# Kernel tuning notes

Measured on AMD Instinct MI355X. Metric: run time of the kernel, lower is better.

## Reference

```python
import jax, jax.numpy as jnp
import numpy as np

NUM_HEADS = 12
DIM = 768
HEAD_DIM = DIM // NUM_HEADS
SCALE = HEAD_DIM ** -0.5
LORA_ALPHA = 1.0


def setup_inputs() -> dict:
    key = jax.random.key(0)
    ks = jax.random.split(key, 9)
    B, H, W = 1, 64, 64
    return {
        "x": jax.random.normal(ks[0], (B, H, W, DIM), jnp.float32),
        "w_qkv": jax.random.normal(ks[1], (3 * DIM, DIM), jnp.float32) * 0.02,
        "b_qkv": jax.random.normal(ks[2], (3 * DIM,), jnp.float32) * 0.02,
        "lora_A": jax.random.normal(ks[3], (12, DIM), jnp.float32) * 0.02,
        "lora_B": jax.random.normal(ks[4], (3 * DIM, 12), jnp.float32) * 0.02,
        "w_proj": jax.random.normal(ks[5], (DIM, DIM), jnp.float32) * 0.02,
        "b_proj": jax.random.normal(ks[6], (DIM,), jnp.float32) * 0.02,
        "rel_pos_h": jax.random.normal(ks[7], (2 * H - 1, HEAD_DIM), jnp.float32) * 0.02,
        "rel_pos_w": jax.random.normal(ks[8], (2 * W - 1, HEAD_DIM), jnp.float32) * 0.02,
    }


def _get_rel_pos(size: int, rel_pos: jnp.ndarray) -> jnp.ndarray:
    # q_size == k_size and rel_pos.shape[0] == 2*size-1, so no interpolation.
    coords = jnp.arange(size)[:, None] - jnp.arange(size)[None, :] + (size - 1)
    return rel_pos[coords]  # [size, size, head_dim]


def reference(x, w_qkv, b_qkv, lora_A, lora_B, w_proj, b_proj, rel_pos_h, rel_pos_w):
    B, H, W, _ = x.shape
    N = H * W
    # LoRA qkv projection: W_eff path = base + alpha * x @ (B A)^T
    qkv = x @ w_qkv.T + b_qkv + LORA_ALPHA * ((x @ lora_A.T) @ lora_B.T)
    qkv = qkv.reshape(B, N, 3, NUM_HEADS, HEAD_DIM)
    qkv = jnp.transpose(qkv, (2, 0, 3, 1, 4)).reshape(3, B * NUM_HEADS, N, HEAD_DIM)
    q, k, v = qkv[0], qkv[1], qkv[2]
    attn = jnp.einsum('bqc,bkc->bqk', q * SCALE, k)  # [B*nh, N, N]
    # decomposed relative position bias
    Rh = _get_rel_pos(H, rel_pos_h)  # [H, H, hd]
    Rw = _get_rel_pos(W, rel_pos_w)  # [W, W, hd]
    r_q = q.reshape(B * NUM_HEADS, H, W, HEAD_DIM)
    rel_h = jnp.einsum('bhwc,hkc->bhwk', r_q, Rh)
    rel_w = jnp.einsum('bhwc,wkc->bhwk', r_q, Rw)
    attn = (attn.reshape(-1, H, W, H, W)
            + rel_h[:, :, :, :, None]
            + rel_w[:, :, :, None, :]).reshape(-1, N, N)
    attn = jax.nn.softmax(attn, axis=-1)
    out = jnp.einsum('bqk,bkc->bqc', attn, v)  # [B*nh, N, hd]
    out = out.reshape(B, NUM_HEADS, H, W, HEAD_DIM)
    out = jnp.transpose(out, (0, 2, 3, 1, 4)).reshape(B, H, W, DIM)
    return out @ w_proj.T + b_proj
```

## Files before the change

kernel.cpp:

```cpp
#include <hip/hip_runtime.h>
#include <stdint.h>


typedef __attribute__((ext_vector_type(4))) float f32x4;
typedef __attribute__((ext_vector_type(16))) float f32x16;
typedef __attribute__((ext_vector_type(4))) float fvec4;
typedef __attribute__((ext_vector_type(8))) short s16x8;
typedef __attribute__((ext_vector_type(4))) short s16x4;
typedef __attribute__((ext_vector_type(4))) unsigned u32x4;

constexpr int NH  = 12;
constexpr int HD  = 64;
constexpr int DIM = 768;
constexpr int N   = 4096;
constexpr int QKV = 2304;
constexpr float LOG2E  = 1.4426950408889634f;
constexpr float SCALE2 = 0.125f * LOG2E;

static __device__ __forceinline__ short f2bf(float f) {
  unsigned u = __builtin_bit_cast(unsigned, f);
  unsigned r = (u + 0x7FFFu + ((u >> 16) & 1u)) >> 16;
  return (short)r;
}
static __device__ __forceinline__ float bf2f(short s) {
  unsigned u = ((unsigned)(unsigned short)s) << 16;
  return __builtin_bit_cast(float, u);
}
static __device__ __forceinline__ unsigned cvt_pk_bf16(float a, float b) {
  unsigned r;
  asm("v_cvt_pk_bf16_f32 %0, %1, %2" : "=v"(r) : "v"(a), "v"(b));
  return r;
}
static __device__ __forceinline__ float ex2(float x) {
  float r;
  asm("v_exp_f32 %0, %1" : "=v"(r) : "v"(x));
  return r;
}
static __device__ __forceinline__ void gload16(const void* g, void* l) {
  __builtin_amdgcn_global_load_lds(
      (const __attribute__((address_space(1))) void*)g,
      (__attribute__((address_space(3))) void*)l, 16, 0, 0);
}

__global__ __launch_bounds__(256) void k_weff(const float* __restrict__ w_qkv,
                                              const float* __restrict__ lora_A,
                                              const float* __restrict__ lora_B,
                                              short* __restrict__ weff) {
  int e = blockIdx.x * 256 + threadIdx.x;
  if (e >= QKV * DIM) return;
  int r = e / DIM, c = e % DIM;
  float acc = w_qkv[e];
#pragma unroll
  for (int t = 0; t < 12; ++t) acc += lora_B[r * 12 + t] * lora_A[t * DIM + c];
  weff[e] = f2bf(acc);
}

__global__ __launch_bounds__(256) void k_x2bf(const float* __restrict__ x,
                                              short* __restrict__ xb) {
  int i = blockIdx.x * 256 + threadIdx.x;
  fvec4 v = *reinterpret_cast<const fvec4*>(x + (size_t)i * 4);
  s16x4 p;
  p[0] = f2bf(v[0]); p[1] = f2bf(v[1]); p[2] = f2bf(v[2]); p[3] = f2bf(v[3]);
  *reinterpret_cast<s16x4*>(xb + (size_t)i * 4) = p;
}

__global__ __launch_bounds__(256) void k_wsplit(const float* __restrict__ w,
                                                short* __restrict__ ws) {
  int r = blockIdx.y;
  int kk = blockIdx.x * 256 + threadIdx.x;
  int blk = (kk >= 1536) ? 2 : (kk >= 768 ? 1 : 0);
  int c = kk - blk * 768;
  float wv = w[(size_t)r * 768 + c];
  short hi = f2bf(wv);
  ws[(size_t)r * 2304 + kk] = (blk == 1) ? f2bf(wv - bf2f(hi)) : hi;
}

template <int KIT, int MODE, int BM>
__global__ __launch_bounds__(256) void k_gemm(const short* __restrict__ A,
                                              const short* __restrict__ B,
                                              const float* __restrict__ bias,
                                              short* __restrict__ qo,
                                              short* __restrict__ ko,
                                              short* __restrict__ vo,
                                              float* __restrict__ outf) {
  constexpr int MFR = BM / 32;
  __shared__ __align__(16) char lds[BM * 128 + 16384];
  const int tid = threadIdx.x;
  const int wave = tid >> 6, lane = tid & 63, lr = lane & 15, lg = lane >> 4;
  const int wr = wave >> 1, wc = wave & 1;
  const int i0 = blockIdx.x * BM, j0 = blockIdx.y * 128;
  const int LDA = KIT * 128;

  size_t offA[MFR], offB[4];
#pragma unroll
  for (int it = 0; it < MFR; ++it) {
    int c = it * 256 + tid;
    int row = c >> 3;
    offA[it] = (size_t)row * LDA + (((c & 7) << 4) ^ ((row & 7) << 4));
  }
#pragma unroll
  for (int it = 0; it < 4; ++it) {
    int c = it * 256 + tid;
    int row = c >> 3;
    offB[it] = (size_t)row * LDA + (((c & 7) << 4) ^ ((row & 7) << 4));
  }
  const char* Ab = (const char*)A + (size_t)i0 * LDA;
  const char* Bb = (const char*)B + (size_t)j0 * LDA;
  char* la = lds + wave * 1024;
  char* lb = lds + BM * 128 + wave * 1024;

  const int swz = (lr & 7) << 4;
  const int ab = (wr * (BM / 2) + lr) * 128 + ((lg * 16) ^ swz);
  const int bb = BM * 128 + (wc * 64 + lr) * 128 + ((lg * 16) ^ swz);

  f32x4 acc[MFR][4] = {};

  for (int kt = 0; kt < KIT; ++kt) {
    const size_t kadd = (size_t)kt * 128;
#pragma unroll
    for (int it = 0; it < MFR; ++it) gload16(Ab + kadd + offA[it], la + it * 4096);
#pragma unroll
    for (int it = 0; it < 4; ++it) gload16(Bb + kadd + offB[it], lb + it * 4096);
    __syncthreads();
#pragma unroll
    for (int ks2 = 0; ks2 < 2; ++ks2) {
      s16x8 af[MFR], bf_[4];
#pragma unroll
      for (int m = 0; m < MFR; ++m)
        af[m] = *reinterpret_cast<const s16x8*>(lds + ((ab + m * 2048) ^ (ks2 << 6)));
#pragma unroll
      for (int n = 0; n < 4; ++n)
        bf_[n] = *reinterpret_cast<const s16x8*>(lds + ((bb + n * 2048) ^ (ks2 << 6)));
#pragma unroll
      for (int m = 0; m < MFR; ++m)
#pragma unroll
        for (int n = 0; n < 4; ++n)
          acc[m][n] = __builtin_amdgcn_mfma_f32_16x16x32_bf16(af[m], bf_[n], acc[m][n], 0, 0, 0);
    }
    __syncthreads();
  }

  if constexpr (MODE == 0) {
    const int three = j0 / 768;
    const int head = ((j0 % 768) >> 6) + wc;
    short* dst = (three == 0) ? qo : ((three == 1) ? ko : vo);
#pragma unroll
    for (int n = 0; n < 4; ++n) {
      const int col = n * 16 + lr;
      const float bj = bias[j0 + wc * 64 + col];
#pragma unroll
      for (int m = 0; m < MFR; ++m)
#pragma unroll
        for (int r = 0; r < 4; ++r) {
          int i = i0 + wr * (BM / 2) + m * 16 + lg * 4 + r;
          dst[((size_t)head * N + i) * HD + col] = f2bf(acc[m][n][r] + bj);
        }
    }
  } else {
#pragma unroll
    for (int n = 0; n < 4; ++n) {
      const int j = j0 + wc * 64 + n * 16 + lr;
      const float bj = bias[j];
#pragma unroll
      for (int m = 0; m < MFR; ++m)
#pragma unroll
        for (int r = 0; r < 4; ++r) {
          int i = i0 + wr * (BM / 2) + m * 16 + lg * 4 + r;
          outf[(size_t)i * 768 + j] = acc[m][n][r] + bj;
        }
    }
  }
}

__global__ __launch_bounds__(256) void k_vT(const short* __restrict__ vg,
                                            short* __restrict__ vTg) {
  __shared__ short ts[64 * 72];
  const int tid = threadIdx.x;
  const int i0 = blockIdx.x * 64;
  const int h = blockIdx.y;
#pragma unroll
  for (int it = 0; it < 2; ++it) {
    int ch = tid + 256 * it;
    int row = ch >> 3, cc = (ch & 7) * 8;
    *reinterpret_cast<s16x8*>(&ts[row * 72 + cc]) =
        *reinterpret_cast<const s16x8*>(&vg[((size_t)h * N + i0 + row) * HD + cc]);
  }
  __syncthreads();
#pragma unroll
  for (int it = 0; it < 2; ++it) {
    int ch = tid + 256 * it;
    int c = ch >> 3, ii = (ch & 7) * 8;
    s16x8 o;
#pragma unroll
    for (int j = 0; j < 8; ++j) o[j] = ts[(ii + j) * 72 + c];
    *reinterpret_cast<s16x8*>(&vTg[((size_t)h * HD + c) * N + i0 + ii]) = o;
  }
}

__global__ __launch_bounds__(256) void k_relh(const short* __restrict__ qg,
                                              const float* __restrict__ tab,
                                              short* __restrict__ rhT) {
  __shared__ short Ts[64 * 72];
  const int tid = threadIdx.x;
  const int wave = tid >> 6, lane = tid & 63, lr = lane & 15, lg = lane >> 4;
  const int h = blockIdx.x >> 6, qh = blockIdx.x & 63;
#pragma unroll
  for (int it = 0; it < 4; ++it) {
    int e = tid + 256 * it;
    int row = e >> 4, c4 = (e & 15) * 4;
    fvec4 v = *reinterpret_cast<const fvec4*>(tab + (size_t)(qh + 63 - row) * 64 + c4);
    s16x4 p;
    p[0] = f2bf(v[0]); p[1] = f2bf(v[1]); p[2] = f2bf(v[2]); p[3] = f2bf(v[3]);
    *reinterpret_cast<s16x4*>(&Ts[row * 72 + c4]) = p;
  }
  __syncthreads();
  const size_t qrow = (size_t)h * N + qh * 64 + wave * 16 + lr;
  const s16x8 a0 = *reinterpret_cast<const s16x8*>(qg + qrow * 64 + lg * 8);
  const s16x8 a1 = *reinterpret_cast<const s16x8*>(qg + qrow * 64 + 32 + lg * 8);
  f32x4 acc[4] = {};
#pragma unroll
  for (int ks2 = 0; ks2 < 2; ++ks2)
#pragma unroll
    for (int n = 0; n < 4; ++n) {
      s16x8 b = *reinterpret_cast<const s16x8*>(&Ts[(n * 16 + lr) * 72 + ks2 * 32 + lg * 8]);
      acc[n] = __builtin_amdgcn_mfma_f32_16x16x32_bf16(ks2 ? a1 : a0, b, acc[n], 0, 0, 0);
    }
  const size_t ob = ((size_t)(h * 64 + qh)) * 4096;
#pragma unroll
  for (int n = 0; n < 4; ++n) {
    s16x4 o;
#pragma unroll
    for (int r = 0; r < 4; ++r) o[r] = f2bf(acc[n][r]);
    *reinterpret_cast<s16x4*>(&rhT[ob + (size_t)(n * 16 + lr) * 64 + wave * 16 + lg * 4]) = o;
  }
}

__global__ __launch_bounds__(256) void k_relw(const short* __restrict__ qg,
                                              const float* __restrict__ tab,
                                              short* __restrict__ rwg) {
  __shared__ short Ts[128 * 72];
  const int tid = threadIdx.x;
  const int wave = tid >> 6, lane = tid & 63, lr = lane & 15, lg = lane >> 4;
  const int h = blockIdx.x >> 6, qh = blockIdx.x & 63;
#pragma unroll
  for (int it = 0; it < 8; ++it) {
    int e = tid + 256 * it;
    int row = e >> 4, c4 = (e & 15) * 4;
    s16x4 p = {0, 0, 0, 0};
    if (row < 127) {
      fvec4 v = *reinterpret_cast<const fvec4*>(tab + (size_t)row * 64 + c4);
      p[0] = f2bf(v[0]); p[1] = f2bf(v[1]); p[2] = f2bf(v[2]); p[3] = f2bf(v[3]);
    }
    *reinterpret_cast<s16x4*>(&Ts[row * 72 + c4]) = p;
  }
  __syncthreads();
  const size_t qrow = (size_t)h * N + qh * 64 + wave * 16 + lr;
  const s16x8 a0 = *reinterpret_cast<const s16x8*>(qg + qrow * 64 + lg * 8);
  const s16x8 a1 = *reinterpret_cast<const s16x8*>(qg + qrow * 64 + 32 + lg * 8);
  f32x4 acc[8] = {};
#pragma unroll
  for (int ks2 = 0; ks2 < 2; ++ks2)
#pragma unroll
    for (int n = 0; n < 8; ++n) {
      s16x8 b = *reinterpret_cast<const s16x8*>(&Ts[(n * 16 + lr) * 72 + ks2 * 32 + lg * 8]);
      acc[n] = __builtin_amdgcn_mfma_f32_16x16x32_bf16(ks2 ? a1 : a0, b, acc[n], 0, 0, 0);
    }
  const size_t ob = ((size_t)h * N + qh * 64) * 64;
#pragma unroll
  for (int n = 0; n < 8; ++n) {
    int d = n * 16 + lr;
#pragma unroll
    for (int r = 0; r < 4; ++r) {
      int qw = wave * 16 + lg * 4 + r;
      int kw = qw + 63 - d;
      if ((unsigned)kw < 64u) rwg[ob + (size_t)qw * 64 + kw] = f2bf(acc[n][r]);
    }
  }
}

__global__ __launch_bounds__(256, 3) void k_flash(const short* __restrict__ qg,
                                                  const short* __restrict__ kg,
                                                  const short* __restrict__ vTg,
                                                  const short* __restrict__ rhTg,
                                                  const short* __restrict__ rwg,
                                                  short* __restrict__ aprime) {
  __shared__ __align__(16) char lds[32768];
  const int tid = threadIdx.x;
  const int wave = tid >> 6, lane = tid & 63;
  const int ql = lane & 31, hi = lane >> 5;
  const int qh2 = wave >> 1, kh2 = wave & 1;
  const int h = blockIdx.x >> 6, qt = blockIdx.x & 63;
  const int i0 = qt * 64;
  const int qglob = i0 + qh2 * 32 + ql;

  const short* qrowp = qg + ((size_t)h * N + qglob) * 64 + hi * 8;
  const s16x8 qb0 = *reinterpret_cast<const s16x8*>(qrowp);
  const s16x8 qb1 = *reinterpret_cast<const s16x8*>(qrowp + 16);
  const s16x8 qb2 = *reinterpret_cast<const s16x8*>(qrowp + 32);
  const s16x8 qb3 = *reinterpret_cast<const s16x8*>(qrowp + 48);

  const short* rwp = rwg + ((size_t)h * N + qglob) * 64 + kh2 * 32 + hi * 4;
  float rw2[16];
#pragma unroll
  for (int reg = 0; reg < 16; ++reg)
    rw2[reg] = LOG2E * bf2f(rwp[(reg & 3) + 8 * (reg >> 2)]);

  const short* rhp = rhTg + ((size_t)(h * 64 + qt)) * 4096 + qh2 * 32 + ql;

  const int c0 = wave * 64 + lane, c1 = c0 + 256;
  const int r0 = c0 >> 3, r1 = c1 >> 3;
  const int sw0 = (((c0 & 7) << 4) ^ ((r0 & 7) << 4));
  const int sw1 = (((c1 & 7) << 4) ^ ((r1 & 7) << 4));
  const char* kgb = (const char*)kg + (size_t)h * N * 128;
  const char* vgb = (const char*)vTg + (size_t)h * 64 * 8192;
  const size_t ko0 = (size_t)r0 * 128 + sw0, ko1 = (size_t)r1 * 128 + sw1;
  const size_t vo0 = (size_t)r0 * 8192 + sw0, vo1 = (size_t)r1 * 8192 + sw1;
  char* lk0 = lds + wave * 1024;
  char* lv0 = lds + 16384 + wave * 1024;

  auto STAGE = [&](int t, int buf) {
    const char* kp = kgb + (size_t)t * 8192;
    const char* vp = vgb + (size_t)t * 128;
    char* lk = lk0 + buf * 8192;
    char* lv = lv0 + buf * 8192;
    gload16(kp + ko0, lk);
    gload16(kp + ko1, lk + 4096);
    gload16(vp + vo0, lv);
    gload16(vp + vo1, lv + 4096);
  };

  const int swz = (ql & 7) << 4;
  const int colb = (hi << 4) ^ swz;
  const int krd = (kh2 * 32 + ql) * 128;

  f32x16 acc0 = {}, acc1 = {};
  float lsum = 0.f;

  STAGE(0, 0);
  __syncthreads();

  for (int t = 0; t < 64; ++t) {
    const int buf = t & 1;
    STAGE(t + 1 < 64 ? t + 1 : 63, buf ^ 1);
    const float rh2 = LOG2E * bf2f(rhp[t * 64]);

    f32x16 sa = {};
    {
      const char* LK = lds + buf * 8192 + krd;
      s16x8 ka0 = *reinterpret_cast<const s16x8*>(LK + (colb ^ 0));
      sa = __builtin_amdgcn_mfma_f32_32x32x16_bf16(ka0, qb0, sa, 0, 0, 0);
      s16x8 ka1 = *reinterpret_cast<const s16x8*>(LK + (colb ^ 32));
      sa = __builtin_amdgcn_mfma_f32_32x32x16_bf16(ka1, qb1, sa, 0, 0, 0);
      s16x8 ka2 = *reinterpret_cast<const s16x8*>(LK + (colb ^ 64));
      sa = __builtin_amdgcn_mfma_f32_32x32x16_bf16(ka2, qb2, sa, 0, 0, 0);
      s16x8 ka3 = *reinterpret_cast<const s16x8*>(LK + (colb ^ 96));
      sa = __builtin_amdgcn_mfma_f32_32x32x16_bf16(ka3, qb3, sa, 0, 0, 0);
    }

    float p[16];
#pragma unroll
    for (int reg = 0; reg < 16; ++reg) {
      p[reg] = ex2(fmaf(sa[reg], SCALE2, rh2 + rw2[reg]));
      lsum += p[reg];
    }

    unsigned w00 = cvt_pk_bf16(p[0], p[1]),   w01 = cvt_pk_bf16(p[2], p[3]);
    unsigned w10 = cvt_pk_bf16(p[4], p[5]),   w11 = cvt_pk_bf16(p[6], p[7]);
    unsigned w20 = cvt_pk_bf16(p[8], p[9]),   w21 = cvt_pk_bf16(p[10], p[11]);
    unsigned w30 = cvt_pk_bf16(p[12], p[13]), w31 = cvt_pk_bf16(p[14], p[15]);
    asm("v_permlane32_swap_b32 %0, %1" : "+v"(w00), "+v"(w10));
    asm("v_permlane32_swap_b32 %0, %1" : "+v"(w01), "+v"(w11));
    asm("v_permlane32_swap_b32 %0, %1" : "+v"(w20), "+v"(w30));
    asm("v_permlane32_swap_b32 %0, %1" : "+v"(w21), "+v"(w31));
    u32x4 u0 = {w00, w01, w10, w11};
    u32x4 u1 = {w20, w21, w30, w31};
    s16x8 pa0 = __builtin_bit_cast(s16x8, u0);
    s16x8 pa1 = __builtin_bit_cast(s16x8, u1);

    {
      const char* LV = lds + 16384 + buf * 8192;
      const int cv0 = (kh2 * 2 + 0) << 5, cv1 = (kh2 * 2 + 1) << 5;
      s16x8 v00 = *reinterpret_cast<const s16x8*>(LV + ql * 128 + (colb ^ cv0));
      acc0 = __builtin_amdgcn_mfma_f32_32x32x16_bf16(pa0, v00, acc0, 0, 0, 0);
      s16x8 v01 = *reinterpret_cast<const s16x8*>(LV + ql * 128 + (colb ^ cv1));
      acc0 = __builtin_amdgcn_mfma_f32_32x32x16_bf16(pa1, v01, acc0, 0, 0, 0);
      s16x8 v10 = *reinterpret_cast<const s16x8*>(LV + 4096 + ql * 128 + (colb ^ cv0));
      acc1 = __builtin_amdgcn_mfma_f32_32x32x16_bf16(pa0, v10, acc1, 0, 0, 0);
      s16x8 v11 = *reinterpret_cast<const s16x8*>(LV + 4096 + ql * 128 + (colb ^ cv1));
      acc1 = __builtin_amdgcn_mfma_f32_32x32x16_bf16(pa1, v11, acc1, 0, 0, 0);
    }
    __syncthreads();
  }

  lsum += __shfl_xor(lsum, 32);
  float* LS = (float*)(lds + 16384);
  float* OF = (float*)lds;
  if (lane < 32) LS[(qh2 * 2 + kh2) * 32 + ql] = lsum;
  if (kh2 == 0) {
#pragma unroll
    for (int reg = 0; reg < 16; ++reg) {
      int qoff = (reg & 3) + 8 * (reg >> 2) + 4 * hi;
      OF[qh2 * 2048 + qoff * 64 + ql] = acc0[reg];
      OF[qh2 * 2048 + qoff * 64 + 32 + ql] = acc1[reg];
    }
  }
  __syncthreads();
  if (kh2 == 1) {
    float invq = 1.0f / (LS[qh2 * 64 + ql] + LS[qh2 * 64 + 32 + ql]);
#pragma unroll
    for (int reg = 0; reg < 16; ++reg) {
      int qoff = (reg & 3) + 8 * (reg >> 2) + 4 * hi;
      float inv = __shfl(invq, qoff);
      size_t rbase = (size_t)(i0 + qh2 * 32 + qoff) * 2304 + h * 64;
#pragma unroll
      for (int ct = 0; ct < 2; ++ct) {
        float o = ((ct ? acc1 : acc0)[reg] + OF[qh2 * 2048 + qoff * 64 + ct * 32 + ql]) * inv;
        short ohi = f2bf(o);
        float lo = o - bf2f(ohi);
        size_t base = rbase + ct * 32 + ql;
        aprime[base] = ohi;
        aprime[base + 768] = ohi;
        aprime[base + 1536] = f2bf(lo);
      }
    }
  }
}

extern "C" void kernel_launch(void* const* d_in, const int* in_sizes, int n_in,
                              void* d_out, int out_size, void* d_ws, size_t ws_size,
                              hipStream_t stream) {
  const float* x      = (const float*)d_in[0];
  const float* w_qkv  = (const float*)d_in[1];
  const float* b_qkv  = (const float*)d_in[2];
  const float* lora_A = (const float*)d_in[3];
  const float* lora_B = (const float*)d_in[4];
  const float* w_proj = (const float*)d_in[5];
  const float* b_proj = (const float*)d_in[6];
  const float* rel_h  = (const float*)d_in[7];
  const float* rel_w  = (const float*)d_in[8];
  float* out = (float*)d_out;

  char* ws = (char*)d_ws;
  short* weff   = (short*)(ws + 0);
  short* xb     = (short*)(ws + 3538944);
  short* vg     = (short*)(ws + 9830400);
  short* aprime = (short*)(ws + 0);
  short* qg     = (short*)(ws + 18874368);
  short* kg     = (short*)(ws + 25165824);
  short* vTg    = (short*)(ws + 31457280);
  short* rhT    = (short*)(ws + 37748736);
  short* rwg    = (short*)(ws + 44040192);
  short* wsp    = (short*)(ws + 50331648);
  (void)ws_size; (void)in_sizes; (void)n_in; (void)out_size;

  k_weff<<<dim3((QKV * DIM + 255) / 256), dim3(256), 0, stream>>>(w_qkv, lora_A, lora_B, weff);
  k_x2bf<<<dim3(3072), dim3(256), 0, stream>>>(x, xb);
  k_wsplit<<<dim3(9, 768), dim3(256), 0, stream>>>(w_proj, wsp);
  k_gemm<12, 0, 128><<<dim3(32, 18), dim3(256), 0, stream>>>(xb, weff, b_qkv, qg, kg, vg, nullptr);
  k_vT<<<dim3(64, NH), dim3(256), 0, stream>>>(vg, vTg);
  k_relh<<<dim3(NH * 64), dim3(256), 0, stream>>>(qg, rel_h, rhT);
  k_relw<<<dim3(NH * 64), dim3(256), 0, stream>>>(qg, rel_w, rwg);
  k_flash<<<dim3(NH * 64), dim3(256), 0, stream>>>(qg, kg, vTg, rhT, rwg, aprime);
  k_gemm<36, 1, 64><<<dim3(64, 6), dim3(256), 0, stream>>>(aprime, wsp, b_proj, nullptr, nullptr, nullptr, out);
}
```

Before: 183.0 us.

## Restructure flash attention to split keys across waves with 128-key tiles

The flash kernel now has each wave own both 32-query halves of the 64-query tile and a separate key slice, instead of splitting queries and keys between wave pairs. It stages 128-key K/V tiles into a doubled 64KB LDS buffer, with two waves loading K and two loading V, and runs 32 iterations instead of 64. The epilogue reduces the four waves' partial outputs through swizzled LDS and writes vectorized bf16 hi/lo stores. It also adds MFMA priority hints, remaps block IDs across heads, and prefetches the rel-pos row. The larger LDS and register footprint lowers occupancy from 3 to 2 blocks per CU, in exchange for fewer barriers and more reuse of loaded K/V fragments.

```diff
diff --git a/kernel.cpp b/kernel.cpp
--- a/kernel.cpp
+++ b/kernel.cpp
@@ -278,152 +278,217 @@
   }
 }
 
-__global__ __launch_bounds__(256, 3) void k_flash(const short* __restrict__ qg,
+#define QG_BLOCK(QB0, QB1, QB2, QB3, RW, RH2, ACC0, ACC1, LA, LB)              \
+  do {                                                                         \
+    f32x16 sa = {};                                                            \
+    __builtin_amdgcn_s_setprio(1);                                             \
+    sa = __builtin_amdgcn_mfma_f32_32x32x16_bf16(kf0, QB0, sa, 0, 0, 0);       \
+    sa = __builtin_amdgcn_mfma_f32_32x32x16_bf16(kf1, QB1, sa, 0, 0, 0);       \
+    sa = __builtin_amdgcn_mfma_f32_32x32x16_bf16(kf2, QB2, sa, 0, 0, 0);       \
+    sa = __builtin_amdgcn_mfma_f32_32x32x16_bf16(kf3, QB3, sa, 0, 0, 0);       \
+    __builtin_amdgcn_s_setprio(0);                                             \
+    float p[16];                                                               \
+    _Pragma("unroll")                                                          \
+    for (int reg = 0; reg < 16; ++reg)                                         \
+      p[reg] = ex2(fmaf(sa[reg], SCALE2, RH2 + RW[reg]));                      \
+    float t0 = (p[0] + p[1]) + (p[2] + p[3]);                                  \
+    float t1 = (p[4] + p[5]) + (p[6] + p[7]);                                  \
+    float t2 = (p[8] + p[9]) + (p[10] + p[11]);                                \
+    float t3 = (p[12] + p[13]) + (p[14] + p[15]);                              \
+    LA += t0 + t1;                                                             \
+    LB += t2 + t3;                                                             \
+    unsigned w00 = cvt_pk_bf16(p[0], p[1]),   w01 = cvt_pk_bf16(p[2], p[3]);   \
+    unsigned w10 = cvt_pk_bf16(p[4], p[5]),   w11 = cvt_pk_bf16(p[6], p[7]);   \
+    unsigned w20 = cvt_pk_bf16(p[8], p[9]),   w21 = cvt_pk_bf16(p[10], p[11]); \
+    unsigned w30 = cvt_pk_bf16(p[12], p[13]), w31 = cvt_pk_bf16(p[14], p[15]); \
+    asm("v_permlane32_swap_b32 %0, %1" : "+v"(w00), "+v"(w10));                \
+    asm("v_permlane32_swap_b32 %0, %1" : "+v"(w01), "+v"(w11));                \
+    asm("v_permlane32_swap_b32 %0, %1" : "+v"(w20), "+v"(w30));                \
+    asm("v_permlane32_swap_b32 %0, %1" : "+v"(w21), "+v"(w31));                \
+    u32x4 u0 = {w00, w01, w10, w11};                                           \
+    u32x4 u1 = {w20, w21, w30, w31};                                           \
+    s16x8 pa0 = __builtin_bit_cast(s16x8, u0);                                 \
+    s16x8 pa1 = __builtin_bit_cast(s16x8, u1);                                 \
+    __builtin_amdgcn_s_setprio(1);                                             \
+    ACC0 = __builtin_amdgcn_mfma_f32_32x32x16_bf16(pa0, vf0, ACC0, 0, 0, 0);   \
+    ACC0 = __builtin_amdgcn_mfma_f32_32x32x16_bf16(pa1, vf2, ACC0, 0, 0, 0);   \
+    ACC1 = __builtin_amdgcn_mfma_f32_32x32x16_bf16(pa0, vf1, ACC1, 0, 0, 0);   \
+    ACC1 = __builtin_amdgcn_mfma_f32_32x32x16_bf16(pa1, vf3, ACC1, 0, 0, 0);   \
+    __builtin_amdgcn_s_setprio(0);                                             \
+  } while (0)
+
+__global__ __launch_bounds__(256, 2) void k_flash(const short* __restrict__ qg,
                                                   const short* __restrict__ kg,
                                                   const short* __restrict__ vTg,
                                                   const short* __restrict__ rhTg,
                                                   const short* __restrict__ rwg,
                                                   short* __restrict__ aprime) {
-  __shared__ __align__(16) char lds[32768];
+  __shared__ __align__(16) char lds[65536];
   const int tid = threadIdx.x;
   const int wave = tid >> 6, lane = tid & 63;
   const int ql = lane & 31, hi = lane >> 5;
-  const int qh2 = wave >> 1, kh2 = wave & 1;
-  const int h = blockIdx.x >> 6, qt = blockIdx.x & 63;
+  const int kt2 = wave & 1, kh2 = wave >> 1;
+  const int bid = blockIdx.x;
+  const int id = (bid & 7) * 96 + (bid >> 3);
+  const int h = id >> 6, qt = id & 63;
   const int i0 = qt * 64;
-  const int qglob = i0 + qh2 * 32 + ql;
-
-  const short* qrowp = qg + ((size_t)h * N + qglob) * 64 + hi * 8;
-  const s16x8 qb0 = *reinterpret_cast<const s16x8*>(qrowp);
-  const s16x8 qb1 = *reinterpret_cast<const s16x8*>(qrowp + 16);
-  const s16x8 qb2 = *reinterpret_cast<const s16x8*>(qrowp + 32);
-  const s16x8 qb3 = *reinterpret_cast<const s16x8*>(qrowp + 48);
-
-  const short* rwp = rwg + ((size_t)h * N + qglob) * 64 + kh2 * 32 + hi * 4;
-  float rw2[16];
-#pragma unroll
-  for (int reg = 0; reg < 16; ++reg)
-    rw2[reg] = LOG2E * bf2f(rwp[(reg & 3) + 8 * (reg >> 2)]);
-
-  const short* rhp = rhTg + ((size_t)(h * 64 + qt)) * 4096 + qh2 * 32 + ql;
-
-  const int c0 = wave * 64 + lane, c1 = c0 + 256;
-  const int r0 = c0 >> 3, r1 = c1 >> 3;
-  const int sw0 = (((c0 & 7) << 4) ^ ((r0 & 7) << 4));
-  const int sw1 = (((c1 & 7) << 4) ^ ((r1 & 7) << 4));
-  const char* kgb = (const char*)kg + (size_t)h * N * 128;
-  const char* vgb = (const char*)vTg + (size_t)h * 64 * 8192;
-  const size_t ko0 = (size_t)r0 * 128 + sw0, ko1 = (size_t)r1 * 128 + sw1;
-  const size_t vo0 = (size_t)r0 * 8192 + sw0, vo1 = (size_t)r1 * 8192 + sw1;
-  char* lk0 = lds + wave * 1024;
-  char* lv0 = lds + 16384 + wave * 1024;
-
-  auto STAGE = [&](int t, int buf) {
-    const char* kp = kgb + (size_t)t * 8192;
-    const char* vp = vgb + (size_t)t * 128;
-    char* lk = lk0 + buf * 8192;
-    char* lv = lv0 + buf * 8192;
-    gload16(kp + ko0, lk);
-    gload16(kp + ko1, lk + 4096);
-    gload16(vp + vo0, lv);
-    gload16(vp + vo1, lv + 4096);
+
+  const short* q0p = qg + ((size_t)h * N + i0 + ql) * 64 + hi * 8;
+  const short* q1p = q0p + 32 * 64;
+  const s16x8 qb00 = *reinterpret_cast<const s16x8*>(q0p);
+  const s16x8 qb01 = *reinterpret_cast<const s16x8*>(q0p + 16);
+  const s16x8 qb02 = *reinterpret_cast<const s16x8*>(q0p + 32);
+  const s16x8 qb03 = *reinterpret_cast<const s16x8*>(q0p + 48);
+  const s16x8 qb10 = *reinterpret_cast<const s16x8*>(q1p);
+  const s16x8 qb11 = *reinterpret_cast<const s16x8*>(q1p + 16);
+  const s16x8 qb12 = *reinterpret_cast<const s16x8*>(q1p + 32);
+  const s16x8 qb13 = *reinterpret_cast<const s16x8*>(q1p + 48);
+
+  f32x16 rw0, rw1;
+  {
+    const short* rwp0 = rwg + ((size_t)h * N + i0 + ql) * 64 + kh2 * 32 + hi * 4;
+    const short* rwp1 = rwp0 + 32 * 64;
+#pragma unroll
+    for (int reg = 0; reg < 16; ++reg) {
+      int o = (reg & 3) + 8 * (reg >> 2);
+      rw0[reg] = LOG2E * bf2f(rwp0[o]);
+      rw1[reg] = LOG2E * bf2f(rwp1[o]);
+    }
+  }
+  const short* rhp = rhTg + ((size_t)(h * 64 + qt)) * 4096;
+
+  int soff[8];
+  const char* sbase;
+  if (wave < 2) {
+    sbase = (const char*)kg + (size_t)h * N * 128 + wave * 64 * 128;
+#pragma unroll
+    for (int it = 0; it < 8; ++it) {
+      int c = it * 64 + lane, row = c >> 3;
+      soff[it] = row * 128 + (((c & 7) << 4) ^ ((row & 7) << 4));
+    }
+  } else {
+    sbase = (const char*)vTg + (size_t)h * 64 * 8192 + (wave - 2) * 128;
+#pragma unroll
+    for (int it = 0; it < 8; ++it) {
+      int c = it * 64 + lane, r = c >> 3;
+      soff[it] = r * 8192 + (((c & 7) << 4) ^ ((r & 7) << 4));
+    }
+  }
+  const int sstep = (wave < 2) ? 16384 : 256;
+  char* lreg = lds + wave * 8192;
+
+  auto STAGE = [&](int i, int buf) {
+    const char* sp = sbase + (size_t)i * sstep;
+    char* lp = lreg + buf * 32768;
+#pragma unroll
+    for (int it = 0; it < 8; ++it) gload16(sp + soff[it], lp + it * 1024);
   };
 
-  const int swz = (ql & 7) << 4;
-  const int colb = (hi << 4) ^ swz;
-  const int krd = (kh2 * 32 + ql) * 128;
-
-  f32x16 acc0 = {}, acc1 = {};
-  float lsum = 0.f;
+  const int swzq = (ql & 7) << 4;
+  const int krow = (kt2 * 64 + kh2 * 32 + ql) * 128;
+  const int kco0 = krow + ((0 * 32 + hi * 16) ^ swzq);
+  const int kco1 = krow + ((1 * 32 + hi * 16) ^ swzq);
+  const int kco2 = krow + ((2 * 32 + hi * 16) ^ swzq);
+  const int kco3 = krow + ((3 * 32 + hi * 16) ^ swzq);
+  const int vrow0 = 16384 + kt2 * 8192 + ql * 128;
+  const int vrow1 = vrow0 + 32 * 128;
+  const int vch0 = (kh2 * 64 + 0 * 32 + hi * 16) ^ swzq;
+  const int vch1 = (kh2 * 64 + 1 * 32 + hi * 16) ^ swzq;
+  const int vco0 = vrow0 + vch0;
+  const int vco1 = vrow1 + vch0;
+  const int vco2 = vrow0 + vch1;
+  const int vco3 = vrow1 + vch1;
+
+  f32x16 acc00 = {}, acc01 = {}, acc10 = {}, acc11 = {};
+  float la0 = 0.f, lb0 = 0.f, la1 = 0.f, lb1 = 0.f;
+
+  unsigned short rhc0 = (unsigned short)rhp[(size_t)kt2 * 64 + ql];
+  unsigned short rhc1 = (unsigned short)rhp[(size_t)kt2 * 64 + 32 + ql];
 
   STAGE(0, 0);
   __syncthreads();
 
-  for (int t = 0; t < 64; ++t) {
-    const int buf = t & 1;
-    STAGE(t + 1 < 64 ? t + 1 : 63, buf ^ 1);
-    const float rh2 = LOG2E * bf2f(rhp[t * 64]);
-
-    f32x16 sa = {};
-    {
-      const char* LK = lds + buf * 8192 + krd;
-      s16x8 ka0 = *reinterpret_cast<const s16x8*>(LK + (colb ^ 0));
-      sa = __builtin_amdgcn_mfma_f32_32x32x16_bf16(ka0, qb0, sa, 0, 0, 0);
-      s16x8 ka1 = *reinterpret_cast<const s16x8*>(LK + (colb ^ 32));
-      sa = __builtin_amdgcn_mfma_f32_32x32x16_bf16(ka1, qb1, sa, 0, 0, 0);
-      s16x8 ka2 = *reinterpret_cast<const s16x8*>(LK + (colb ^ 64));
-      sa = __builtin_amdgcn_mfma_f32_32x32x16_bf16(ka2, qb2, sa, 0, 0, 0);
-      s16x8 ka3 = *reinterpret_cast<const s16x8*>(LK + (colb ^ 96));
-      sa = __builtin_amdgcn_mfma_f32_32x32x16_bf16(ka3, qb3, sa, 0, 0, 0);
-    }
-
-    float p[16];
-#pragma unroll
-    for (int reg = 0; reg < 16; ++reg) {
-      p[reg] = ex2(fmaf(sa[reg], SCALE2, rh2 + rw2[reg]));
-      lsum += p[reg];
-    }
-
-    unsigned w00 = cvt_pk_bf16(p[0], p[1]),   w01 = cvt_pk_bf16(p[2], p[3]);
-    unsigned w10 = cvt_pk_bf16(p[4], p[5]),   w11 = cvt_pk_bf16(p[6], p[7]);
-    unsigned w20 = cvt_pk_bf16(p[8], p[9]),   w21 = cvt_pk_bf16(p[10], p[11]);
-    unsigned w30 = cvt_pk_bf16(p[12], p[13]), w31 = cvt_pk_bf16(p[14], p[15]);
-    asm("v_permlane32_swap_b32 %0, %1" : "+v"(w00), "+v"(w10));
-    asm("v_permlane32_swap_b32 %0, %1" : "+v"(w01), "+v"(w11));
-    asm("v_permlane32_swap_b32 %0, %1" : "+v"(w20), "+v"(w30));
-    asm("v_permlane32_swap_b32 %0, %1" : "+v"(w21), "+v"(w31));
-    u32x4 u0 = {w00, w01, w10, w11};
-    u32x4 u1 = {w20, w21, w30, w31};
-    s16x8 pa0 = __builtin_bit_cast(s16x8, u0);
-    s16x8 pa1 = __builtin_bit_cast(s16x8, u1);
-
-    {
-      const char* LV = lds + 16384 + buf * 8192;
-      const int cv0 = (kh2 * 2 + 0) << 5, cv1 = (kh2 * 2 + 1) << 5;
-      s16x8 v00 = *reinterpret_cast<const s16x8*>(LV + ql * 128 + (colb ^ cv0));
-      acc0 = __builtin_amdgcn_mfma_f32_32x32x16_bf16(pa0, v00, acc0, 0, 0, 0);
-      s16x8 v01 = *reinterpret_cast<const s16x8*>(LV + ql * 128 + (colb ^ cv1));
-      acc0 = __builtin_amdgcn_mfma_f32_32x32x16_bf16(pa1, v01, acc0, 0, 0, 0);
-      s16x8 v10 = *reinterpret_cast<const s16x8*>(LV + 4096 + ql * 128 + (colb ^ cv0));
-      acc1 = __builtin_amdgcn_mfma_f32_32x32x16_bf16(pa0, v10, acc1, 0, 0, 0);
-      s16x8 v11 = *reinterpret_cast<const s16x8*>(LV + 4096 + ql * 128 + (colb ^ cv1));
-      acc1 = __builtin_amdgcn_mfma_f32_32x32x16_bf16(pa1, v11, acc1, 0, 0, 0);
-    }
+  for (int i = 0; i < 32; ++i) {
+    const int buf = i & 1;
+    if (i + 1 < 32) STAGE(i + 1, buf ^ 1);
+    const int nx = (i + 1 < 32) ? i + 1 : 31;
+    unsigned short rhn0 = (unsigned short)rhp[(size_t)(nx * 2 + kt2) * 64 + ql];
+    unsigned short rhn1 = (unsigned short)rhp[(size_t)(nx * 2 + kt2) * 64 + 32 + ql];
+
+    const char* bufp = lds + buf * 32768;
+    s16x8 kf0 = *reinterpret_cast<const s16x8*>(bufp + kco0);
+    s16x8 kf1 = *reinterpret_cast<const s16x8*>(bufp + kco1);
+    s16x8 kf2 = *reinterpret_cast<const s16x8*>(bufp + kco2);
+    s16x8 kf3 = *reinterpret_cast<const s16x8*>(bufp + kco3);
+    s16x8 vf0 = *reinterpret_cast<const s16x8*>(bufp + vco0);
+    s16x8 vf1 = *reinterpret_cast<const s16x8*>(bufp + vco1);
+    s16x8 vf2 = *reinterpret_cast<const s16x8*>(bufp + vco2);
+    s16x8 vf3 = *reinterpret_cast<const s16x8*>(bufp + vco3);
+
+    const float rh20 = LOG2E * bf2f((short)rhc0);
+    const float rh21 = LOG2E * bf2f((short)rhc1);
+
+    QG_BLOCK(qb00, qb01, qb02, qb03, rw0, rh20, acc00, acc01, la0, lb0);
+    QG_BLOCK(qb10, qb11, qb12, qb13, rw1, rh21, acc10, acc11, la1, lb1);
+
+    rhc0 = rhn0; rhc1 = rhn1;
     __syncthreads();
   }
 
-  lsum += __shfl_xor(lsum, 32);
-  float* LS = (float*)(lds + 16384);
+  float l0 = la0 + lb0, l1 = la1 + lb1;
+  l0 += __shfl_xor(l0, 32);
+  l1 += __shfl_xor(l1, 32);
+  float* LS = (float*)lds;
+  if (lane < 32) {
+    LS[wave * 64 + ql] = l0;
+    LS[wave * 64 + 32 + ql] = l1;
+  }
+  __syncthreads();
+  const int eq = wave * 16 + (lane >> 2);
+  const int cb = (lane & 3) * 16;
+  float inv = 1.0f / (LS[eq] + LS[64 + eq] + LS[128 + eq] + LS[192 + eq]);
+  __syncthreads();
   float* OF = (float*)lds;
-  if (lane < 32) LS[(qh2 * 2 + kh2) * 32 + ql] = lsum;
-  if (kh2 == 0) {
-#pragma unroll
-    for (int reg = 0; reg < 16; ++reg) {
-      int qoff = (reg & 3) + 8 * (reg >> 2) + 4 * hi;
-      OF[qh2 * 2048 + qoff * 64 + ql] = acc0[reg];
-      OF[qh2 * 2048 + qoff * 64 + 32 + ql] = acc1[reg];
-    }
-  }
-  __syncthreads();
-  if (kh2 == 1) {
-    float invq = 1.0f / (LS[qh2 * 64 + ql] + LS[qh2 * 64 + 32 + ql]);
-#pragma unroll
-    for (int reg = 0; reg < 16; ++reg) {
-      int qoff = (reg & 3) + 8 * (reg >> 2) + 4 * hi;
-      float inv = __shfl(invq, qoff);
-      size_t rbase = (size_t)(i0 + qh2 * 32 + qoff) * 2304 + h * 64;
-#pragma unroll
-      for (int ct = 0; ct < 2; ++ct) {
-        float o = ((ct ? acc1 : acc0)[reg] + OF[qh2 * 2048 + qoff * 64 + ct * 32 + ql]) * inv;
-        short ohi = f2bf(o);
-        float lo = o - bf2f(ohi);
-        size_t base = rbase + ct * 32 + ql;
-        aprime[base] = ohi;
-        aprime[base + 768] = ohi;
-        aprime[base + 1536] = f2bf(lo);
+#pragma unroll
+  for (int qg2 = 0; qg2 < 2; ++qg2)
+#pragma unroll
+    for (int ct = 0; ct < 2; ++ct) {
+      const f32x16& a = qg2 ? (ct ? acc11 : acc10) : (ct ? acc01 : acc00);
+#pragma unroll
+      for (int reg = 0; reg < 16; ++reg) {
+        int q = qg2 * 32 + (reg & 3) + 8 * (reg >> 2) + 4 * hi;
+        int c = ct * 32 + ql;
+        OF[wave * 4096 + q * 64 + (c ^ ((q & 7) << 2))] = a[reg];
       }
     }
-  }
+  __syncthreads();
+  f32x4 osum[4] = {};
+#pragma unroll
+  for (int w = 0; w < 4; ++w)
+#pragma unroll
+    for (int j = 0; j < 4; ++j)
+      osum[j] += *reinterpret_cast<const f32x4*>(
+          &OF[w * 4096 + eq * 64 + ((cb + j * 4) ^ ((eq & 7) << 2))]);
+
+  s16x8 hi8[2], lo8[2];
+#pragma unroll
+  for (int j = 0; j < 4; ++j)
+#pragma unroll
+    for (int e = 0; e < 4; ++e) {
+      float o = osum[j][e] * inv;
+      short oh = f2bf(o);
+      float lo = o - bf2f(oh);
+      int idx = j * 4 + e;
+      hi8[idx >> 3][idx & 7] = oh;
+      lo8[idx >> 3][idx & 7] = f2bf(lo);
+    }
+  size_t obase = (size_t)(i0 + eq) * 2304 + h * 64 + cb;
+  *reinterpret_cast<s16x8*>(&aprime[obase]) = hi8[0];
+  *reinterpret_cast<s16x8*>(&aprime[obase + 8]) = hi8[1];
+  *reinterpret_cast<s16x8*>(&aprime[obase + 768]) = hi8[0];
+  *reinterpret_cast<s16x8*>(&aprime[obase + 776]) = hi8[1];
+  *reinterpret_cast<s16x8*>(&aprime[obase + 1536]) = lo8[0];
+  *reinterpret_cast<s16x8*>(&aprime[obase + 1544]) = lo8[1];
 }
 
 extern "C" void kernel_launch(void* const* d_in, const int* in_sizes, int n_in,
```

New measurement: 179.8 us. Within noise of the previous version (-1.7%).
